# Performance work log

Measured on AMD Instinct MI355X. Metric: run time of the kernel, lower is better.

The kernel has to match this reference:

```python
import jax, jax.numpy as jnp
import numpy as np
import math

N_HEAD = 4
NORM_GROUPS = 16
EPS = 1e-5


def setup_inputs() -> dict:
    key = jax.random.key(0)
    ks = jax.random.split(key, 4)
    B, C, H, W = 2, 256, 64, 64
    return {
        "input": jax.random.normal(ks[0], (B, C, H, W), dtype=jnp.float32),
        "gn_weight": jnp.ones((C,), dtype=jnp.float32),
        "gn_bias": jnp.zeros((C,), dtype=jnp.float32),
        # 1x1 convs are plain channel matmuls: weight [out_ch, in_ch]
        "qkv_weight": jax.random.normal(ks[1], (3 * C, C), dtype=jnp.float32) / math.sqrt(C),
        "out_weight": jax.random.normal(ks[2], (C, C), dtype=jnp.float32) / math.sqrt(C),
        "out_bias": jnp.zeros((C,), dtype=jnp.float32),
    }


def _group_norm(x, weight, bias):
    B, C, H, W = x.shape
    g = x.reshape(B, NORM_GROUPS, C // NORM_GROUPS, H, W)
    mu = g.mean(axis=(2, 3, 4), keepdims=True)
    var = g.var(axis=(2, 3, 4), keepdims=True)
    g = (g - mu) * jax.lax.rsqrt(var + EPS)
    return g.reshape(B, C, H, W) * weight[:, None, None] + bias[:, None, None]


def reference(input, gn_weight, gn_bias, qkv_weight, out_weight, out_bias):
    B, C, H, W = input.shape
    head_dim = C // N_HEAD
    x = _group_norm(input, gn_weight, gn_bias)
    # 1x1 conv (no bias) -> [B, 3C, H, W] -> [B, n_head, 3*head_dim, H, W]
    qkv = jnp.einsum('bchw,oc->bohw', x, qkv_weight)
    qkv = qkv.reshape(B, N_HEAD, 3 * head_dim, H, W)
    q, k, v = jnp.split(qkv, 3, axis=2)
    # full spatial attention; note: scale is sqrt(channel), as in the source
    attn = jnp.einsum('bnchw,bncyx->bnhwyx', q, k) / math.sqrt(C)
    attn = jax.nn.softmax(attn.reshape(B, N_HEAD, H, W, H * W), axis=-1)
    attn = attn.reshape(B, N_HEAD, H, W, H, W)
    out = jnp.einsum('bnhwyx,bncyx->bnchw', attn, v).reshape(B, C, H, W)
    out = jnp.einsum('bchw,oc->bohw', out, out_weight) + out_bias[:, None, None]
    return out + input
```

## Files before the change

### kernel.cpp

```cpp
#include <hip/hip_runtime.h>

typedef __bf16        bf16x8 __attribute__((ext_vector_type(8)));
typedef float         f32x4  __attribute__((ext_vector_type(4)));
typedef unsigned short u16x4 __attribute__((ext_vector_type(4)));
typedef unsigned int  u32x4  __attribute__((ext_vector_type(4)));

#define MFMA16(a,b,c) __builtin_amdgcn_mfma_f32_16x16x32_bf16((a),(b),(c),0,0,0)

static __device__ __forceinline__ unsigned short f2bf(float f) {
  unsigned int u = __builtin_bit_cast(unsigned int, f);
  u += 0x7fffu + ((u >> 16) & 1u);
  return (unsigned short)(u >> 16);
}
static __device__ __forceinline__ unsigned int pk2(float a, float b) {
  unsigned int ua = __builtin_bit_cast(unsigned int, a) + 0x8000u;
  unsigned int ub = __builtin_bit_cast(unsigned int, b) + 0x8000u;
  return __builtin_amdgcn_perm(ub, ua, 0x07060302u);
}
static __device__ __forceinline__ unsigned int pk2rne(float a, float b) {
  return (unsigned int)f2bf(a) | ((unsigned int)f2bf(b) << 16);
}
static __device__ __forceinline__ bf16x8 as_bf(u32x4 v) {
  return __builtin_bit_cast(bf16x8, v);
}

#define SDIM 4096
#define CDIM 256
#define NHEAD 4
#define HDIM 64
#define NBATCH 2

__global__ __launch_bounds__(256) void k_cast_w(const float* __restrict__ wq,
                                                const float* __restrict__ wo,
                                                unsigned short* __restrict__ wqb,
                                                unsigned short* __restrict__ wob) {
  int t = blockIdx.x * 256 + threadIdx.x;
  int i = t * 4;
  u16x4 r;
  if (i < 768 * 256) {
    float4 v = *(const float4*)(wq + i);
    r[0] = f2bf(v.x); r[1] = f2bf(v.y); r[2] = f2bf(v.z); r[3] = f2bf(v.w);
    *(u16x4*)(wqb + i) = r;
  } else {
    int j = i - 768 * 256;
    float4 v = *(const float4*)(wo + j);
    r[0] = f2bf(v.x); r[1] = f2bf(v.y); r[2] = f2bf(v.z); r[3] = f2bf(v.w);
    *(u16x4*)(wob + j) = r;
  }
}

__global__ __launch_bounds__(256) void k_gn_stats(const float* __restrict__ x,
                                                  float2* __restrict__ stats) {
  int bg = blockIdx.x;
  int i  = threadIdx.x;
  const float* p = x + (size_t)bg * 65536;
  float s = 0.f, sq = 0.f;
#pragma unroll 4
  for (int r = 0; r < 64; ++r) {
    float4 v = *(const float4*)(p + (r * 256 + i) * 4);
    s  += v.x + v.y + v.z + v.w;
    sq += v.x * v.x + v.y * v.y + v.z * v.z + v.w * v.w;
  }
  __shared__ float rs[256], rq[256];
  rs[i] = s; rq[i] = sq;
  __syncthreads();
  for (int off = 128; off > 0; off >>= 1) {
    if (i < off) { rs[i] += rs[i + off]; rq[i] += rq[i + off]; }
    __syncthreads();
  }
  if (i == 0) {
    float mean = rs[0] * (1.f / 65536.f);
    float var  = rq[0] * (1.f / 65536.f) - mean * mean;
    stats[bg] = make_float2(mean, rsqrtf(var + 1e-5f));
  }
}

__global__ __launch_bounds__(256) void k_gn_apply(const float* __restrict__ x,
                                                  const float2* __restrict__ stats,
                                                  const float* __restrict__ gnw,
                                                  const float* __restrict__ gnb,
                                                  unsigned short* __restrict__ xn) {
  __shared__ __attribute__((aligned(16))) unsigned short sT[64 * 268];
  int b = blockIdx.y, s0 = blockIdx.x * 64;
  int i = threadIdx.x, lane = i & 63, w = i >> 6;
#pragma unroll 4
  for (int r = 0; r < 64; ++r) {
    int c = r * 4 + w;
    int s = s0 + lane;
    float v = x[((size_t)(b * CDIM + c)) * SDIM + s];
    float2 st = stats[b * 16 + (c >> 4)];
    float nv = (v - st.x) * st.y * gnw[c] + gnb[c];
    sT[lane * 268 + c] = f2bf(nv);
  }
  __syncthreads();
#pragma unroll
  for (int r = 0; r < 16; ++r) {
    int sl = r * 4 + w;
    u16x4 v = *(const u16x4*)&sT[sl * 268 + lane * 4];
    *(u16x4*)&xn[((size_t)(b * SDIM + s0 + sl)) * CDIM + lane * 4] = v;
  }
}

template <int M, int MODE>
__global__ __launch_bounds__(256) void k_gemm(const unsigned short* __restrict__ W,
                                              const unsigned short* __restrict__ X,
                                              unsigned short* __restrict__ outQ,
                                              unsigned short* __restrict__ outK,
                                              unsigned short* __restrict__ outV,
                                              float* __restrict__ outf,
                                              const float* __restrict__ bias,
                                              const float* __restrict__ resid) {
  __shared__ __attribute__((aligned(16))) unsigned short sX[64 * 40];
  int b = blockIdx.z, s0 = blockIdx.y * 64, o0 = blockIdx.x * 64;
  int i = threadIdx.x, lane = i & 63, w = i >> 6;
  int quad = lane >> 4, m = lane & 15;
  const unsigned short* Xb = X + ((size_t)b * SDIM + s0) * CDIM;
  int ss = i >> 2, cq = i & 3;

  f32x4 acc[4] = {};
#pragma unroll
  for (int k0 = 0; k0 < 256; k0 += 32) {
    u32x4 xv = *(const u32x4*)(Xb + ss * CDIM + k0 + cq * 8);
    *(u32x4*)&sX[ss * 40 + cq * 8] = xv;
    __syncthreads();
    bf16x8 a = as_bf(*(const u32x4*)(W + (o0 + w * 16 + m) * 256 + k0 + quad * 8));
#pragma unroll
    for (int st = 0; st < 4; ++st) {
      bf16x8 bx = as_bf(*(const u32x4*)&sX[(st * 16 + m) * 40 + quad * 8]);
      acc[st] = MFMA16(a, bx, acc[st]);
    }
    __syncthreads();
  }
  if (MODE == 1) {
#pragma unroll
    for (int st = 0; st < 4; ++st)
#pragma unroll
      for (int r = 0; r < 4; ++r) {
        int o = o0 + w * 16 + quad * 4 + r;
        int s = s0 + st * 16 + m;
        size_t idx = ((size_t)b * M + o) * SDIM + s;
        outf[idx] = acc[st][r] + bias[o] + resid[idx];
      }
  } else {
    int sec = (o0 >> 6) % 3;
    int h   = o0 / 192;
    int bh  = b * NHEAD + h;
    if (sec == 2) {
#pragma unroll
      for (int st = 0; st < 4; ++st)
#pragma unroll
        for (int r = 0; r < 4; ++r) {
          int d = w * 16 + quad * 4 + r;
          int s = s0 + st * 16 + m;
          outV[((size_t)bh * HDIM + d) * SDIM + s] = f2bf(acc[st][r]);
        }
    } else {
      unsigned short* dst = (sec == 0) ? outQ : outK;
      float qs = (sec == 0) ? 0.09016844f : 1.0f;
#pragma unroll
      for (int st = 0; st < 4; ++st) {
        int s = s0 + st * 16 + m;
        size_t base = ((size_t)bh * SDIM + s) * HDIM + w * 16 + quad * 4;
        *(unsigned int*)(dst + base)     = pk2rne(acc[st][0] * qs, acc[st][1] * qs);
        *(unsigned int*)(dst + base + 2) = pk2rne(acc[st][2] * qs, acc[st][3] * qs);
      }
    }
  }
}

__global__ __launch_bounds__(256, 2) void k_attn(const unsigned short* __restrict__ Qt,
                                                 const unsigned short* __restrict__ Kt,
                                                 const unsigned short* __restrict__ Vb,
                                                 unsigned short* __restrict__ ao) {
  __shared__ __attribute__((aligned(16))) char smem[20480];
  __shared__ float libuf[4][64];
  int b = blockIdx.z, h = blockIdx.y, q0 = blockIdx.x * 64;
  int bh = b * NHEAD + h;
  int i = threadIdx.x, lane = i & 63, w = i >> 6;
  int quad = lane >> 4, m = lane & 15;

  const unsigned short* Qr = Qt + ((size_t)bh * SDIM + q0 + m) * HDIM + quad * 8;
  const unsigned short* Kr = Kt + ((size_t)bh * SDIM + m) * HDIM + quad * 8;
  const unsigned short* Vr = Vb + ((size_t)bh * HDIM + m) * SDIM + quad * 8;
  char* Pw = smem + w * 5120;

  bf16x8 bq[4][2];
#pragma unroll
  for (int qt = 0; qt < 4; ++qt)
#pragma unroll
    for (int ks = 0; ks < 2; ++ks)
      bq[qt][ks] = as_bf(*(const u32x4*)(Qr + qt * 16 * HDIM + ks * 32));

  f32x4 oacc[4][4] = {};
  float li[4] = {0.f, 0.f, 0.f, 0.f};

  int kbase = w * (SDIM / 4);
  for (int kt0 = 0; kt0 < SDIM / 4; kt0 += 32) {
    int kt = kbase + kt0;
    bf16x8 ak[2][2];
#pragma unroll
    for (int ky = 0; ky < 2; ++ky)
#pragma unroll
      for (int ks = 0; ks < 2; ++ks)
        ak[ky][ks] = as_bf(*(const u32x4*)(Kr + (size_t)(kt + ky * 16) * HDIM + ks * 32));
    bf16x8 av[4];
#pragma unroll
    for (int dt = 0; dt < 4; ++dt)
      av[dt] = as_bf(*(const u32x4*)(Vr + (size_t)dt * 16 * SDIM + kt));

#pragma unroll
    for (int qt = 0; qt < 4; ++qt) {
      f32x4 sc0 = {-18.f, -18.f, -18.f, -18.f};
      f32x4 sc1 = sc0;
      sc0 = MFMA16(ak[0][0], bq[qt][0], sc0);
      sc0 = MFMA16(ak[0][1], bq[qt][1], sc0);
      sc1 = MFMA16(ak[1][0], bq[qt][0], sc1);
      sc1 = MFMA16(ak[1][1], bq[qt][1], sc1);
      float p[8];
#pragma unroll
      for (int r = 0; r < 4; ++r) {
        p[r]     = __builtin_amdgcn_exp2f(sc0[r]);
        p[4 + r] = __builtin_amdgcn_exp2f(sc1[r]);
      }
      li[qt] += ((p[0] + p[1]) + (p[2] + p[3])) + ((p[4] + p[5]) + (p[6] + p[7]));
      char* pb = Pw + qt * 1280 + m * 80 + quad * 8;
      *(uint2*)(pb)      = make_uint2(pk2(p[0], p[1]), pk2(p[2], p[3]));
      *(uint2*)(pb + 32) = make_uint2(pk2(p[4], p[5]), pk2(p[6], p[7]));
    }
#pragma unroll
    for (int qt = 0; qt < 4; ++qt) {
      bf16x8 bp = *(bf16x8*)(Pw + qt * 1280 + m * 80 + quad * 16);
#pragma unroll
      for (int dt = 0; dt < 4; ++dt)
        oacc[qt][dt] = MFMA16(av[dt], bp, oacc[qt][dt]);
    }
  }

#pragma unroll
  for (int qt = 0; qt < 4; ++qt) {
    li[qt] += __shfl_xor(li[qt], 16);
    li[qt] += __shfl_xor(li[qt], 32);
  }
  if (quad == 0) {
#pragma unroll
    for (int qt = 0; qt < 4; ++qt) libuf[w][qt * 16 + m] = li[qt];
  }
  __syncthreads();

  float* obuf = (float*)smem;
#pragma unroll
  for (int pw = 0; pw < 4; ++pw) {
    if (w == pw) {
#pragma unroll
      for (int qt = 0; qt < 4; ++qt)
#pragma unroll
        for (int dt = 0; dt < 4; ++dt) {
          float* dst = obuf + (qt * 16 + m) * 68 + dt * 16 + quad * 4;
          f32x4 v = oacc[qt][dt];
          if (pw > 0) v = v + *(f32x4*)dst;
          *(f32x4*)dst = v;
        }
    }
    __syncthreads();
  }

  {
    int q = i & 63, dg = i >> 6;
    float lsum = libuf[0][q] + libuf[1][q] + libuf[2][q] + libuf[3][q];
    float linv = 1.f / lsum;
    const float* src = obuf + q * 68 + dg * 16;
    unsigned int dw[8];
#pragma unroll
    for (int e = 0; e < 8; ++e) dw[e] = pk2rne(src[2 * e] * linv, src[2 * e + 1] * linv);
    unsigned short* dst = ao + ((size_t)b * SDIM + q0 + q) * CDIM + h * HDIM + dg * 16;
    *(u32x4*)(dst)     = u32x4{dw[0], dw[1], dw[2], dw[3]};
    *(u32x4*)(dst + 8) = u32x4{dw[4], dw[5], dw[6], dw[7]};
  }
}

extern "C" void kernel_launch(void* const* d_in, const int* in_sizes, int n_in,
                              void* d_out, int out_size, void* d_ws, size_t ws_size,
                              hipStream_t stream) {
  const float* input = (const float*)d_in[0];
  const float* gnw   = (const float*)d_in[1];
  const float* gnb   = (const float*)d_in[2];
  const float* wq    = (const float*)d_in[3];
  const float* wo    = (const float*)d_in[4];
  const float* ob    = (const float*)d_in[5];
  float* out = (float*)d_out;

  char* ws = (char*)d_ws;
  unsigned short* xn  = (unsigned short*)(ws);
  unsigned short* Qt  = (unsigned short*)(ws + (4ull  << 20));
  unsigned short* Kt  = (unsigned short*)(ws + (8ull  << 20));
  unsigned short* Vb  = (unsigned short*)(ws + (12ull << 20));
  unsigned short* ao  = (unsigned short*)(ws + (16ull << 20));
  unsigned short* wqb = (unsigned short*)(ws + (20ull << 20));
  unsigned short* wob = (unsigned short*)(ws + (20ull << 20) + (1u << 19));
  float2* stats       = (float2*)(ws + (21ull << 20));

  k_cast_w<<<256, 256, 0, stream>>>(wq, wo, wqb, wob);
  k_gn_stats<<<32, 256, 0, stream>>>(input, stats);
  k_gn_apply<<<dim3(64, NBATCH), 256, 0, stream>>>(input, stats, gnw, gnb, xn);
  k_gemm<768, 0><<<dim3(12, 64, NBATCH), 256, 0, stream>>>(wqb, xn, Qt, Kt, Vb, nullptr, nullptr, nullptr);
  k_attn<<<dim3(64, NHEAD, NBATCH), 256, 0, stream>>>(Qt, Kt, Vb, ao);
  k_gemm<256, 1><<<dim3(4, 64, NBATCH), 256, 0, stream>>>(wob, ao, nullptr, nullptr, nullptr, out, ob, input);
}
```

Measured before the change: 171.8 us.

## Split attention over key ranges with LDS-staged fragment-layout K/V and combine pass

```diff
diff --git a/kernel.cpp b/kernel.cpp
--- a/kernel.cpp
+++ b/kernel.cpp
@@ -3,6 +3,7 @@
 typedef __bf16        bf16x8 __attribute__((ext_vector_type(8)));
 typedef float         f32x4  __attribute__((ext_vector_type(4)));
 typedef unsigned short u16x4 __attribute__((ext_vector_type(4)));
+typedef unsigned short u16x8 __attribute__((ext_vector_type(8)));
 typedef unsigned int  u32x4  __attribute__((ext_vector_type(4)));
 
 #define MFMA16(a,b,c) __builtin_amdgcn_mfma_f32_16x16x32_bf16((a),(b),(c),0,0,0)
@@ -22,6 +23,13 @@
 }
 static __device__ __forceinline__ bf16x8 as_bf(u32x4 v) {
   return __builtin_bit_cast(bf16x8, v);
+}
+static __device__ __forceinline__ float bf2f(unsigned short u) {
+  return __builtin_bit_cast(float, ((unsigned int)u) << 16);
+}
+static __device__ __forceinline__ void dma16(const unsigned short* g, unsigned short* l) {
+  __builtin_amdgcn_global_load_lds((const __attribute__((address_space(1))) unsigned int*)g,
+                                   (__attribute__((address_space(3))) unsigned int*)l, 16, 0, 0);
 }
 
 #define SDIM 4096
@@ -29,66 +37,73 @@
 #define NHEAD 4
 #define HDIM 64
 #define NBATCH 2
-
-__global__ __launch_bounds__(256) void k_cast_w(const float* __restrict__ wq,
-                                                const float* __restrict__ wo,
-                                                unsigned short* __restrict__ wqb,
-                                                unsigned short* __restrict__ wob) {
-  int t = blockIdx.x * 256 + threadIdx.x;
-  int i = t * 4;
-  u16x4 r;
-  if (i < 768 * 256) {
-    float4 v = *(const float4*)(wq + i);
-    r[0] = f2bf(v.x); r[1] = f2bf(v.y); r[2] = f2bf(v.z); r[3] = f2bf(v.w);
-    *(u16x4*)(wqb + i) = r;
+#define KSPLIT 4
+
+__global__ __launch_bounds__(256) void k_prep(const float* __restrict__ x,
+                                              const float* __restrict__ wq,
+                                              const float* __restrict__ wo,
+                                              unsigned short* __restrict__ wqb,
+                                              unsigned short* __restrict__ wob,
+                                              float2* __restrict__ Sp) {
+  int j = blockIdx.x, i = threadIdx.x;
+  if (j < 256) {
+    const float* p = x + (size_t)(j >> 3) * 65536 + (size_t)(j & 7) * 8192;
+    float s = 0.f, sq = 0.f;
+#pragma unroll
+    for (int r = 0; r < 8; ++r) {
+      float4 v = *(const float4*)(p + (r * 256 + i) * 4);
+      s  += v.x + v.y + v.z + v.w;
+      sq += v.x * v.x + v.y * v.y + v.z * v.z + v.w * v.w;
+    }
+    __shared__ float rs[256], rq[256];
+    rs[i] = s; rq[i] = sq;
+    __syncthreads();
+    for (int off = 128; off > 0; off >>= 1) {
+      if (i < off) { rs[i] += rs[i + off]; rq[i] += rq[i + off]; }
+      __syncthreads();
+    }
+    if (i == 0) Sp[j] = make_float2(rs[0], rq[0]);
   } else {
-    int j = i - 768 * 256;
-    float4 v = *(const float4*)(wo + j);
-    r[0] = f2bf(v.x); r[1] = f2bf(v.y); r[2] = f2bf(v.z); r[3] = f2bf(v.w);
-    *(u16x4*)(wob + j) = r;
-  }
-}
-
-__global__ __launch_bounds__(256) void k_gn_stats(const float* __restrict__ x,
-                                                  float2* __restrict__ stats) {
-  int bg = blockIdx.x;
-  int i  = threadIdx.x;
-  const float* p = x + (size_t)bg * 65536;
-  float s = 0.f, sq = 0.f;
-#pragma unroll 4
-  for (int r = 0; r < 64; ++r) {
-    float4 v = *(const float4*)(p + (r * 256 + i) * 4);
-    s  += v.x + v.y + v.z + v.w;
-    sq += v.x * v.x + v.y * v.y + v.z * v.z + v.w * v.w;
-  }
-  __shared__ float rs[256], rq[256];
-  rs[i] = s; rq[i] = sq;
-  __syncthreads();
-  for (int off = 128; off > 0; off >>= 1) {
-    if (i < off) { rs[i] += rs[i + off]; rq[i] += rq[i + off]; }
-    __syncthreads();
-  }
-  if (i == 0) {
-    float mean = rs[0] * (1.f / 65536.f);
-    float var  = rq[0] * (1.f / 65536.f) - mean * mean;
-    stats[bg] = make_float2(mean, rsqrtf(var + 1e-5f));
+    int t = (j - 256) * 256 + i;
+    int e = t * 16;
+#pragma unroll
+    for (int c = 0; c < 4; ++c) {
+      int idx = e + c * 4;
+      const float* src = (idx < 768 * 256) ? (wq + idx) : (wo + idx - 768 * 256);
+      unsigned short* dst = (idx < 768 * 256) ? (wqb + idx) : (wob + idx - 768 * 256);
+      float4 v = *(const float4*)src;
+      u16x4 r; r[0] = f2bf(v.x); r[1] = f2bf(v.y); r[2] = f2bf(v.z); r[3] = f2bf(v.w);
+      *(u16x4*)dst = r;
+    }
   }
 }
 
 __global__ __launch_bounds__(256) void k_gn_apply(const float* __restrict__ x,
-                                                  const float2* __restrict__ stats,
+                                                  const float2* __restrict__ Sp,
                                                   const float* __restrict__ gnw,
                                                   const float* __restrict__ gnb,
                                                   unsigned short* __restrict__ xn) {
   __shared__ __attribute__((aligned(16))) unsigned short sT[64 * 268];
+  __shared__ float2 sStat[16];
   int b = blockIdx.y, s0 = blockIdx.x * 64;
   int i = threadIdx.x, lane = i & 63, w = i >> 6;
+  if (i < 16) {
+    float s = 0.f, sq = 0.f;
+#pragma unroll
+    for (int u = 0; u < 8; ++u) {
+      float2 v = Sp[(b * 16 + i) * 8 + u];
+      s += v.x; sq += v.y;
+    }
+    float mean = s * (1.f / 65536.f);
+    float var  = sq * (1.f / 65536.f) - mean * mean;
+    sStat[i] = make_float2(mean, rsqrtf(var + 1e-5f));
+  }
+  __syncthreads();
 #pragma unroll 4
   for (int r = 0; r < 64; ++r) {
     int c = r * 4 + w;
-    int s = s0 + lane;
-    float v = x[((size_t)(b * CDIM + c)) * SDIM + s];
-    float2 st = stats[b * 16 + (c >> 4)];
+    float v = x[((size_t)(b * CDIM + c)) * SDIM + s0 + lane];
+    float2 st = sStat[c >> 4];
     float nv = (v - st.x) * st.y * gnw[c] + gnb[c];
     sT[lane * 268 + c] = f2bf(nv);
   }
@@ -104,13 +119,14 @@
 template <int M, int MODE>
 __global__ __launch_bounds__(256) void k_gemm(const unsigned short* __restrict__ W,
                                               const unsigned short* __restrict__ X,
-                                              unsigned short* __restrict__ outQ,
-                                              unsigned short* __restrict__ outK,
-                                              unsigned short* __restrict__ outV,
+                                              unsigned short* __restrict__ Qf,
+                                              unsigned short* __restrict__ Kf,
+                                              unsigned short* __restrict__ Vf,
                                               float* __restrict__ outf,
                                               const float* __restrict__ bias,
                                               const float* __restrict__ resid) {
   __shared__ __attribute__((aligned(16))) unsigned short sX[64 * 40];
+  __shared__ __attribute__((aligned(16))) unsigned short sB[64 * 68];
   int b = blockIdx.z, s0 = blockIdx.y * 64, o0 = blockIdx.x * 64;
   int i = threadIdx.x, lane = i & 63, w = i >> 6;
   int quad = lane >> 4, m = lane & 15;
@@ -145,68 +161,90 @@
     int sec = (o0 >> 6) % 3;
     int h   = o0 / 192;
     int bh  = b * NHEAD + h;
-    if (sec == 2) {
-#pragma unroll
-      for (int st = 0; st < 4; ++st)
-#pragma unroll
-        for (int r = 0; r < 4; ++r) {
-          int d = w * 16 + quad * 4 + r;
-          int s = s0 + st * 16 + m;
-          outV[((size_t)bh * HDIM + d) * SDIM + s] = f2bf(acc[st][r]);
-        }
+    float qs = (sec == 0) ? 0.09016844f : 1.0f;
+#pragma unroll
+    for (int st = 0; st < 4; ++st) {
+      uint2 pk = make_uint2(pk2rne(acc[st][0] * qs, acc[st][1] * qs),
+                            pk2rne(acc[st][2] * qs, acc[st][3] * qs));
+      *(uint2*)&sB[(st * 16 + m) * 68 + w * 16 + quad * 4] = pk;
+    }
+    __syncthreads();
+    int lp = i & 63, qp = lp >> 4, mp = lp & 15, t = i >> 6;
+    if (sec < 2) {
+      unsigned short* base = (sec == 0) ? Qf : Kf;
+#pragma unroll
+      for (int ks = 0; ks < 2; ++ks) {
+        const unsigned short* src = &sB[(t * 16 + mp) * 68 + ks * 32 + qp * 8];
+        u16x4 lo = *(const u16x4*)src;
+        u16x4 hi = *(const u16x4*)(src + 4);
+        unsigned short* dst = base + ((((size_t)bh * 256 + (s0 >> 4) + t) * 2 + ks) * 64 + lp) * 8;
+        *(u16x4*)dst = lo;
+        *(u16x4*)(dst + 4) = hi;
+      }
     } else {
-      unsigned short* dst = (sec == 0) ? outQ : outK;
-      float qs = (sec == 0) ? 0.09016844f : 1.0f;
-#pragma unroll
-      for (int st = 0; st < 4; ++st) {
-        int s = s0 + st * 16 + m;
-        size_t base = ((size_t)bh * SDIM + s) * HDIM + w * 16 + quad * 4;
-        *(unsigned int*)(dst + base)     = pk2rne(acc[st][0] * qs, acc[st][1] * qs);
-        *(unsigned int*)(dst + base + 2) = pk2rne(acc[st][2] * qs, acc[st][3] * qs);
+      int kt32l = t >> 1, dts = (t & 1) * 2;
+#pragma unroll
+      for (int dd = 0; dd < 2; ++dd) {
+        int dt = dts + dd;
+        u16x8 v;
+#pragma unroll
+        for (int jj = 0; jj < 8; ++jj)
+          v[jj] = sB[(kt32l * 32 + qp * 8 + jj) * 68 + dt * 16 + mp];
+        unsigned short* dst = Vf + ((((size_t)bh * 128 + (s0 >> 5) + kt32l) * 4 + dt) * 64 + lp) * 8;
+        *(u16x8*)dst = v;
       }
     }
   }
 }
 
-__global__ __launch_bounds__(256, 2) void k_attn(const unsigned short* __restrict__ Qt,
-                                                 const unsigned short* __restrict__ Kt,
-                                                 const unsigned short* __restrict__ Vb,
-                                                 unsigned short* __restrict__ ao) {
-  __shared__ __attribute__((aligned(16))) char smem[20480];
-  __shared__ float libuf[4][64];
-  int b = blockIdx.z, h = blockIdx.y, q0 = blockIdx.x * 64;
-  int bh = b * NHEAD + h;
+__global__ __launch_bounds__(256, 2) void k_attn(const unsigned short* __restrict__ Qf,
+                                                 const unsigned short* __restrict__ Kf,
+                                                 const unsigned short* __restrict__ Vf,
+                                                 unsigned short* __restrict__ Opb,
+                                                 float* __restrict__ Lp) {
+  __shared__ __attribute__((aligned(16))) unsigned short sK[2][2048];
+  __shared__ __attribute__((aligned(16))) unsigned short sV[2][2048];
+  __shared__ __attribute__((aligned(16))) unsigned short sP[4][64 * 40];
+  int bh = blockIdx.y, kk = blockIdx.z;
   int i = threadIdx.x, lane = i & 63, w = i >> 6;
   int quad = lane >> 4, m = lane & 15;
-
-  const unsigned short* Qr = Qt + ((size_t)bh * SDIM + q0 + m) * HDIM + quad * 8;
-  const unsigned short* Kr = Kt + ((size_t)bh * SDIM + m) * HDIM + quad * 8;
-  const unsigned short* Vr = Vb + ((size_t)bh * HDIM + m) * SDIM + quad * 8;
-  char* Pw = smem + w * 5120;
+  int qbase = blockIdx.x * 256 + w * 64;
 
   bf16x8 bq[4][2];
 #pragma unroll
   for (int qt = 0; qt < 4; ++qt)
 #pragma unroll
     for (int ks = 0; ks < 2; ++ks)
-      bq[qt][ks] = as_bf(*(const u32x4*)(Qr + qt * 16 * HDIM + ks * 32));
+      bq[qt][ks] = as_bf(*(const u32x4*)(Qf +
+        ((((size_t)bh * 256 + ((qbase >> 4) + qt)) * 2 + ks) * 64 + lane) * 8));
 
   f32x4 oacc[4][4] = {};
   float li[4] = {0.f, 0.f, 0.f, 0.f};
 
-  int kbase = w * (SDIM / 4);
-  for (int kt0 = 0; kt0 < SDIM / 4; kt0 += 32) {
-    int kt = kbase + kt0;
-    bf16x8 ak[2][2];
+  auto dma = [&](int it, int buf) {
+    int kb16 = kk * 64 + it * 2 + (w >> 1);
+    dma16(Kf + ((((size_t)bh * 256 + kb16) * 2 + (w & 1)) * 64 + lane) * 8,
+          &sK[buf][w * 512]);
+    int kb32 = kk * 32 + it;
+    dma16(Vf + ((((size_t)bh * 128 + kb32) * 4 + w) * 64 + lane) * 8,
+          &sV[buf][w * 512]);
+  };
+  dma(0, 0);
+
+  for (int it = 0; it < 32; ++it) {
+    int buf = it & 1;
+    __syncthreads();
+    if (it < 31) dma(it + 1, buf ^ 1);
+
+    bf16x8 ak[2][2], av[4];
 #pragma unroll
     for (int ky = 0; ky < 2; ++ky)
 #pragma unroll
       for (int ks = 0; ks < 2; ++ks)
-        ak[ky][ks] = as_bf(*(const u32x4*)(Kr + (size_t)(kt + ky * 16) * HDIM + ks * 32));
-    bf16x8 av[4];
+        ak[ky][ks] = *(const bf16x8*)&sK[buf][((ky * 2 + ks) * 64 + lane) * 8];
 #pragma unroll
     for (int dt = 0; dt < 4; ++dt)
-      av[dt] = as_bf(*(const u32x4*)(Vr + (size_t)dt * 16 * SDIM + kt));
+      av[dt] = *(const bf16x8*)&sV[buf][(dt * 64 + lane) * 8];
 
 #pragma unroll
     for (int qt = 0; qt < 4; ++qt) {
@@ -223,19 +261,20 @@
         p[4 + r] = __builtin_amdgcn_exp2f(sc1[r]);
       }
       li[qt] += ((p[0] + p[1]) + (p[2] + p[3])) + ((p[4] + p[5]) + (p[6] + p[7]));
-      char* pb = Pw + qt * 1280 + m * 80 + quad * 8;
-      *(uint2*)(pb)      = make_uint2(pk2(p[0], p[1]), pk2(p[2], p[3]));
-      *(uint2*)(pb + 32) = make_uint2(pk2(p[4], p[5]), pk2(p[6], p[7]));
+      int row = (qt * 16 + m) * 40;
+      *(uint2*)&sP[w][row + quad * 4]      = make_uint2(pk2(p[0], p[1]), pk2(p[2], p[3]));
+      *(uint2*)&sP[w][row + 16 + quad * 4] = make_uint2(pk2(p[4], p[5]), pk2(p[6], p[7]));
     }
 #pragma unroll
     for (int qt = 0; qt < 4; ++qt) {
-      bf16x8 bp = *(bf16x8*)(Pw + qt * 1280 + m * 80 + quad * 16);
+      bf16x8 bp = *(const bf16x8*)&sP[w][(qt * 16 + m) * 40 + quad * 8];
 #pragma unroll
       for (int dt = 0; dt < 4; ++dt)
         oacc[qt][dt] = MFMA16(av[dt], bp, oacc[qt][dt]);
     }
   }
 
+  size_t qg = (size_t)(kk * 8 + bh) * SDIM + qbase;
 #pragma unroll
   for (int qt = 0; qt < 4; ++qt) {
     li[qt] += __shfl_xor(li[qt], 16);
@@ -243,39 +282,42 @@
   }
   if (quad == 0) {
 #pragma unroll
-    for (int qt = 0; qt < 4; ++qt) libuf[w][qt * 16 + m] = li[qt];
-  }
-  __syncthreads();
-
-  float* obuf = (float*)smem;
-#pragma unroll
-  for (int pw = 0; pw < 4; ++pw) {
-    if (w == pw) {
-#pragma unroll
-      for (int qt = 0; qt < 4; ++qt)
-#pragma unroll
-        for (int dt = 0; dt < 4; ++dt) {
-          float* dst = obuf + (qt * 16 + m) * 68 + dt * 16 + quad * 4;
-          f32x4 v = oacc[qt][dt];
-          if (pw > 0) v = v + *(f32x4*)dst;
-          *(f32x4*)dst = v;
-        }
-    }
-    __syncthreads();
-  }
-
-  {
-    int q = i & 63, dg = i >> 6;
-    float lsum = libuf[0][q] + libuf[1][q] + libuf[2][q] + libuf[3][q];
-    float linv = 1.f / lsum;
-    const float* src = obuf + q * 68 + dg * 16;
-    unsigned int dw[8];
-#pragma unroll
-    for (int e = 0; e < 8; ++e) dw[e] = pk2rne(src[2 * e] * linv, src[2 * e + 1] * linv);
-    unsigned short* dst = ao + ((size_t)b * SDIM + q0 + q) * CDIM + h * HDIM + dg * 16;
-    *(u32x4*)(dst)     = u32x4{dw[0], dw[1], dw[2], dw[3]};
-    *(u32x4*)(dst + 8) = u32x4{dw[4], dw[5], dw[6], dw[7]};
-  }
+    for (int qt = 0; qt < 4; ++qt) Lp[qg + qt * 16 + m] = li[qt];
+  }
+#pragma unroll
+  for (int qt = 0; qt < 4; ++qt)
+#pragma unroll
+    for (int dt = 0; dt < 4; ++dt) {
+      uint2 pk = make_uint2(pk2rne(oacc[qt][dt][0], oacc[qt][dt][1]),
+                            pk2rne(oacc[qt][dt][2], oacc[qt][dt][3]));
+      *(uint2*)&Opb[(qg + qt * 16 + m) * 64 + dt * 16 + quad * 4] = pk;
+    }
+}
+
+__global__ __launch_bounds__(256) void k_combine(const unsigned short* __restrict__ Opb,
+                                                 const float* __restrict__ Lp,
+                                                 unsigned short* __restrict__ ao) {
+  int gid = blockIdx.x * 256 + threadIdx.x;
+  int bh = gid >> 14, rem = gid & 16383, q = rem >> 2, dq = rem & 3;
+  float li = 0.f, o[16];
+#pragma unroll
+  for (int e = 0; e < 16; ++e) o[e] = 0.f;
+#pragma unroll
+  for (int ks = 0; ks < KSPLIT; ++ks) {
+    size_t base = (size_t)(ks * 8 + bh) * SDIM + q;
+    li += Lp[base];
+    const unsigned short* p = Opb + base * 64 + dq * 16;
+    u16x8 a = *(const u16x8*)p, b2 = *(const u16x8*)(p + 8);
+#pragma unroll
+    for (int e = 0; e < 8; ++e) { o[e] += bf2f(a[e]); o[8 + e] += bf2f(b2[e]); }
+  }
+  float inv = 1.f / li;
+  unsigned int dw[8];
+#pragma unroll
+  for (int e = 0; e < 8; ++e) dw[e] = pk2rne(o[2 * e] * inv, o[2 * e + 1] * inv);
+  unsigned short* dst = ao + ((size_t)((bh >> 2) * SDIM + q)) * CDIM + (bh & 3) * HDIM + dq * 16;
+  *(u32x4*)dst       = u32x4{dw[0], dw[1], dw[2], dw[3]};
+  *(u32x4*)(dst + 8) = u32x4{dw[4], dw[5], dw[6], dw[7]};
 }
 
 extern "C" void kernel_launch(void* const* d_in, const int* in_sizes, int n_in,
@@ -291,18 +333,20 @@
 
   char* ws = (char*)d_ws;
   unsigned short* xn  = (unsigned short*)(ws);
-  unsigned short* Qt  = (unsigned short*)(ws + (4ull  << 20));
-  unsigned short* Kt  = (unsigned short*)(ws + (8ull  << 20));
-  unsigned short* Vb  = (unsigned short*)(ws + (12ull << 20));
+  unsigned short* Qf  = (unsigned short*)(ws + (4ull  << 20));
+  unsigned short* Kf  = (unsigned short*)(ws + (8ull  << 20));
+  unsigned short* Vf  = (unsigned short*)(ws + (12ull << 20));
   unsigned short* ao  = (unsigned short*)(ws + (16ull << 20));
   unsigned short* wqb = (unsigned short*)(ws + (20ull << 20));
   unsigned short* wob = (unsigned short*)(ws + (20ull << 20) + (1u << 19));
-  float2* stats       = (float2*)(ws + (21ull << 20));
-
-  k_cast_w<<<256, 256, 0, stream>>>(wq, wo, wqb, wob);
-  k_gn_stats<<<32, 256, 0, stream>>>(input, stats);
-  k_gn_apply<<<dim3(64, NBATCH), 256, 0, stream>>>(input, stats, gnw, gnb, xn);
-  k_gemm<768, 0><<<dim3(12, 64, NBATCH), 256, 0, stream>>>(wqb, xn, Qt, Kt, Vb, nullptr, nullptr, nullptr);
-  k_attn<<<dim3(64, NHEAD, NBATCH), 256, 0, stream>>>(Qt, Kt, Vb, ao);
+  float2* Sp          = (float2*)(ws + (21ull << 20));
+  float* Lp           = (float*)(ws + (21ull << 20) + (1u << 19));
+  unsigned short* Opb = (unsigned short*)(ws + (22ull << 20));
+
+  k_prep<<<320, 256, 0, stream>>>(input, wq, wo, wqb, wob, Sp);
+  k_gn_apply<<<dim3(64, NBATCH), 256, 0, stream>>>(input, Sp, gnw, gnb, xn);
+  k_gemm<768, 0><<<dim3(12, 64, NBATCH), 256, 0, stream>>>(wqb, xn, Qf, Kf, Vf, nullptr, nullptr, nullptr);
+  k_attn<<<dim3(16, NHEAD * NBATCH, KSPLIT), 256, 0, stream>>>(Qf, Kf, Vf, Opb, Lp);
+  k_combine<<<512, 256, 0, stream>>>(Opb, Lp, ao);
   k_gemm<256, 1><<<dim3(4, 64, NBATCH), 256, 0, stream>>>(wob, ao, nullptr, nullptr, nullptr, out, ob, input);
 }
```

After: 159.4 us. -7.2%, faster.
